# Kernel tuning notes

Hardware: AMD Instinct MI355X
Metric: run time of the kernel (lower is better)

The kernel has to match this reference:

```python
import jax, jax.numpy as jnp
import numpy as np

N = 50000      # nodes
E = 800000     # edges (avg degree 16)
F_IN = 128     # input features
HID = 64       # hidden per head
HEADS = 4      # heads per layer
G = 256        # graphs in batch
C = 10         # classes
ALPHA = 0.01   # leaky relu negative slope


def setup_inputs() -> dict:
    key = jax.random.key(0)
    ks = jax.random.split(key, 12)
    x = jax.random.normal(ks[0], (N, F_IN), dtype=jnp.float32)
    edge_index = jax.random.randint(ks[1], (2, E), 0, N, dtype=jnp.int32)
    batch = jnp.sort(jax.random.randint(ks[2], (N,), 0, G, dtype=jnp.int32))

    def glorot(k, shape):
        fan_in = shape[0] if len(shape) == 2 else int(np.prod(shape[1:]))
        return (jax.random.normal(k, shape, dtype=jnp.float32) / np.float32(np.sqrt(fan_in)))

    W1 = glorot(ks[3], (F_IN, HEADS * HID))
    a1_src = glorot(ks[4], (HEADS, HID))
    a1_dst = glorot(ks[5], (HEADS, HID))
    W2 = glorot(ks[6], (HEADS * HID, HEADS * HID))
    a2_src = glorot(ks[7], (HEADS, HID))
    a2_dst = glorot(ks[8], (HEADS, HID))
    lin_W = glorot(ks[9], (2 * HEADS * HID, C))
    lin_b = jnp.zeros((C,), dtype=jnp.float32)
    return {
        "x": x, "edge_index": edge_index, "batch": batch,
        "W1": W1, "a1_src": a1_src, "a1_dst": a1_dst,
        "W2": W2, "a2_src": a2_src, "a2_dst": a2_dst,
        "lin_W": lin_W, "lin_b": lin_b,
    }


def _gat_layer(x, src, dst, W, a_src, a_dst):
    """Multi-head GAT layer: edge softmax over incoming neighbors, concat heads, ELU."""
    n = x.shape[0]
    h, f = a_src.shape
    Wh = (x @ W).reshape(n, h, f)                       # [N,H,F]
    # per-node attention logits (decomposed GAT attention a^T [Wh_i || Wh_j])
    ls = jnp.einsum("nhf,hf->nh", Wh, a_src)            # [N,H]
    ld = jnp.einsum("nhf,hf->nh", Wh, a_dst)            # [N,H]
    e = jax.nn.leaky_relu(ls[src] + ld[dst], ALPHA)      # [E,H]
    # numerically-stable softmax over edges grouped by destination node
    m = jax.ops.segment_max(e, dst, num_segments=n)      # [N,H]
    m = jnp.where(jnp.isfinite(m), m, 0.0)
    p = jnp.exp(e - m[dst])                              # [E,H]
    z = jax.ops.segment_sum(p, dst, num_segments=n)      # [N,H]
    attn = p / (z[dst] + 1e-16)                          # [E,H]
    msg = Wh[src] * attn[:, :, None]                     # [E,H,F]
    out = jax.ops.segment_sum(msg, dst, num_segments=n)  # [N,H,F]
    return jax.nn.elu(out.reshape(n, h * f))


def reference(x, edge_index, batch, W1, a1_src, a1_dst, W2, a2_src, a2_dst, lin_W, lin_b):
    src, dst = edge_index[0], edge_index[1]
    x = _gat_layer(x, src, dst, W1, a1_src, a1_dst)
    x = _gat_layer(x, src, dst, W2, a2_src, a2_dst)
    # global max / mean pool per graph
    mx = jax.ops.segment_max(x, batch, num_segments=G)
    mx = jnp.where(jnp.isfinite(mx), mx, 0.0)
    s = jax.ops.segment_sum(x, batch, num_segments=G)
    cnt = jax.ops.segment_sum(jnp.ones((x.shape[0], 1), x.dtype), batch, num_segments=G)
    mean = s / jnp.maximum(cnt, 1.0)
    pooled = jnp.concatenate([mx, mean], axis=1)         # [G, 2*H*F]
    return pooled @ lin_W + lin_b                        # [G, C]
```

## Files before the change

### kernel.cpp

```cpp
#include <hip/hip_runtime.h>
#include <hip/hip_bf16.h>

#define NNODES 50000
#define NEDGES 800000
#define FIN    128
#define HID    64
#define HEADS  4
#define NGRAPH 256
#define NCLS   10
#define DTOT   256
#define ALPHA  0.01f
#define CAPLG  6
#define CAP    (1 << CAPLG)

typedef short bf16x8 __attribute__((ext_vector_type(8)));
typedef float f32x4  __attribute__((ext_vector_type(4)));

#define NB      ((NNODES + 255) / 256)
#define EB      ((NEDGES + 255) / 256)
#define XB      ((NNODES * FIN / 4 + 255) / 256)
#define W1B     (FIN * DTOT / 256)
#define W2B     (DTOT * DTOT / 256)

__device__ __forceinline__ ushort f2bf(float v) {
    return __bfloat16_as_ushort(__float2bfloat16(v));
}
__device__ __forceinline__ float blo(unsigned u) { return __uint_as_float(u << 16); }
__device__ __forceinline__ float bhi(unsigned u) { return __uint_as_float(u & 0xffff0000u); }
__device__ __forceinline__ unsigned pack2(float lo, float hi) {
    return ((unsigned)f2bf(hi) << 16) | (unsigned)f2bf(lo);
}

__global__ __launch_bounds__(256) void k_setup(const int* __restrict__ src, const int* __restrict__ dst,
                                               int* __restrict__ cursor, ushort* __restrict__ esrc,
                                               const int* __restrict__ batch, int* __restrict__ gstart,
                                               const float4* __restrict__ x4, ushort4* __restrict__ xbf4,
                                               const float* __restrict__ W1, ushort* __restrict__ W1t,
                                               const float* __restrict__ W2, ushort* __restrict__ W2t) {
    int b = blockIdx.x, t = threadIdx.x;
    if (b < EB) {
        int e = b * 256 + t;
        if (e < NEDGES) {
            int d = dst[e];
            int pos = atomicAdd(&cursor[d], 1);
            if (pos < CAP) esrc[(d << CAPLG) + pos] = (ushort)src[e];
        }
    } else if (b < EB + NB) {
        int i = (b - EB) * 256 + t;
        if (i >= NNODES) return;
        int bb = batch[i];
        if (i == 0) {
            for (int g = 0; g <= bb; ++g) gstart[g] = 0;
        } else {
            int pb = batch[i - 1];
            if (pb != bb) for (int g = pb + 1; g <= bb; ++g) gstart[g] = i;
        }
        if (i == NNODES - 1)
            for (int g = bb + 1; g <= NGRAPH; ++g) gstart[g] = NNODES;
    } else if (b < EB + NB + XB) {
        int i = (b - EB - NB) * 256 + t;
        if (i >= NNODES * FIN / 4) return;
        float4 v = x4[i];
        ushort4 o;
        o.x = f2bf(v.x); o.y = f2bf(v.y); o.z = f2bf(v.z); o.w = f2bf(v.w);
        xbf4[i] = o;
    } else if (b < EB + NB + XB + W1B) {
        int id = (b - EB - NB - XB) * 256 + t;
        int n = id & 255, k = id >> 8;
        W1t[n * FIN + (((k >> 3) ^ (n & 7)) << 3) + (k & 7)] = f2bf(W1[k * DTOT + n]);
    } else {
        int id = (b - EB - NB - XB - W1B) * 256 + t;
        int n = id & 255, k = id >> 8;
        W2t[n * DTOT + (((k >> 3) ^ (n & 7)) << 3) + (k & 7)] = f2bf(W2[k * DTOT + n]);
    }
}

template <int K>
__global__ __launch_bounds__(512) void k_gemm_mfma(const ushort* __restrict__ Abf,
                                                   const ushort* __restrict__ Bt,
                                                   ushort* __restrict__ Cbf,
                                                   float* __restrict__ ls,
                                                   float* __restrict__ ld_,
                                                   const float* __restrict__ a_src,
                                                   const float* __restrict__ a_dst,
                                                   int M) {
    __shared__ ushort Bl[256 * 64];
    const int tid  = threadIdx.x;
    const int w    = tid >> 6;
    const int lane = tid & 63;
    const int l15  = lane & 15;
    const int quad = lane >> 4;
    const int m0 = blockIdx.x * 128;

    f32x4 acc[16];
#pragma unroll
    for (int nf = 0; nf < 16; ++nf) acc[nf] = (f32x4){0.f, 0.f, 0.f, 0.f};

    int rowA0 = m0 + w * 16 + l15;  if (rowA0 >= M) rowA0 = M - 1;
    const ushort* pa0 = Abf + (size_t)rowA0 * K + quad * 8;

#pragma unroll
    for (int kc = 0; kc < K / 64; ++kc) {
        {
#pragma unroll
            for (int idx = tid; idx < 2048; idx += 512) {
                int n = idx >> 3, c8 = (idx ^ n) & 7;
                *(uint4*)&Bl[n * 64 + c8 * 8] =
                    *(const uint4*)&Bt[(size_t)n * K + kc * 64 + c8 * 8];
            }
        }
        __syncthreads();
#pragma unroll
        for (int ks = 0; ks < 2; ++ks) {
            bf16x8 a0 = *(const bf16x8*)(pa0 + kc * 64 + ks * 32);
#pragma unroll
            for (int nh = 0; nh < 4; ++nh) {
                bf16x8 bfr[4];
#pragma unroll
                for (int j = 0; j < 4; ++j) {
                    int n = (nh * 4 + j) * 16 + l15;
                    int c = (ks * 4 + quad) ^ (n & 7);
                    bfr[j] = *(const bf16x8*)&Bl[n * 64 + (c << 3)];
                }
#pragma unroll
                for (int j = 0; j < 4; ++j)
                    acc[nh * 4 + j] = __builtin_amdgcn_mfma_f32_16x16x32_bf16(a0, bfr[j], acc[nh * 4 + j], 0, 0, 0);
            }
        }
        __syncthreads();
    }

    float as[16], ad[16];
#pragma unroll
    for (int nf = 0; nf < 16; ++nf) {
        int head = nf >> 2;
        as[nf] = a_src[head * HID + (nf & 3) * 16 + l15];
        ad[nf] = a_dst[head * HID + (nf & 3) * 16 + l15];
    }
#pragma unroll
    for (int reg = 0; reg < 4; ++reg) {
        int row = m0 + w * 16 + quad * 4 + reg;
        bool ok = row < M;
        if (ok) {
#pragma unroll
            for (int nf = 0; nf < 16; ++nf)
                Cbf[(size_t)row * DTOT + nf * 16 + l15] = f2bf(acc[nf][reg]);
        }
        float sh[4], dh[4];
#pragma unroll
        for (int head = 0; head < 4; ++head) {
            float s = 0.f, d = 0.f;
#pragma unroll
            for (int j = 0; j < 4; ++j) {
                int nf = head * 4 + j;
                s += acc[nf][reg] * as[nf];
                d += acc[nf][reg] * ad[nf];
            }
            sh[head] = s; dh[head] = d;
        }
#pragma unroll
        for (int off = 1; off < 16; off <<= 1) {
#pragma unroll
            for (int head = 0; head < 4; ++head) {
                sh[head] += __shfl_xor(sh[head], off);
                dh[head] += __shfl_xor(dh[head], off);
            }
        }
        if (ok && l15 == 0) {
#pragma unroll
            for (int head = 0; head < 4; ++head) {
                ls[row * HEADS + head]  = sh[head];
                ld_[row * HEADS + head] = dh[head];
            }
        }
    }
}

__global__ __launch_bounds__(256) void k_gat_aggr(const int* __restrict__ cnt,
                                                  const ushort* __restrict__ esrc,
                                                  const ushort* __restrict__ Whbf,
                                                  const float* __restrict__ ls,
                                                  const float* __restrict__ ld_,
                                                  ushort* __restrict__ out) {
    const int wv   = threadIdx.x >> 6;
    const int lane = threadIdx.x & 63;
    const int i    = blockIdx.x * 4 + wv;
    if (i >= NNODES) return;
    const int half = lane >> 5;
    const int l32  = lane & 31;
    const int h    = l32 >> 3;
    const int e0 = i << CAPLG;
    int deg = cnt[i]; if (deg > CAP) deg = CAP;
    const int e1 = e0 + deg;
    const float ldv = ld_[i * HEADS + h];

    float ac[8] = {};
    float z = 0.f;
    const int ch = 8 * l32;
    int e = e0 + half;
    for (; e + 6 < e1; e += 8) {
        int s0 = (int)esrc[e], s1 = (int)esrc[e + 2], s2 = (int)esrc[e + 4], s3 = (int)esrc[e + 6];
        float l0 = ls[s0 * HEADS + h] + ldv;
        float l1 = ls[s1 * HEADS + h] + ldv;
        float l2 = ls[s2 * HEADS + h] + ldv;
        float l3 = ls[s3 * HEADS + h] + ldv;
        uint4 u0 = *(const uint4*)&Whbf[(size_t)s0 * DTOT + ch];
        uint4 u1 = *(const uint4*)&Whbf[(size_t)s1 * DTOT + ch];
        uint4 u2 = *(const uint4*)&Whbf[(size_t)s2 * DTOT + ch];
        uint4 u3 = *(const uint4*)&Whbf[(size_t)s3 * DTOT + ch];
        float p0 = __expf(l0 > 0.f ? l0 : ALPHA * l0);
        float p1 = __expf(l1 > 0.f ? l1 : ALPHA * l1);
        float p2 = __expf(l2 > 0.f ? l2 : ALPHA * l2);
        float p3 = __expf(l3 > 0.f ? l3 : ALPHA * l3);
        z += p0 + p1 + p2 + p3;
        ac[0] = fmaf(p0, blo(u0.x), ac[0]); ac[1] = fmaf(p0, bhi(u0.x), ac[1]);
        ac[2] = fmaf(p0, blo(u0.y), ac[2]); ac[3] = fmaf(p0, bhi(u0.y), ac[3]);
        ac[4] = fmaf(p0, blo(u0.z), ac[4]); ac[5] = fmaf(p0, bhi(u0.z), ac[5]);
        ac[6] = fmaf(p0, blo(u0.w), ac[6]); ac[7] = fmaf(p0, bhi(u0.w), ac[7]);
        ac[0] = fmaf(p1, blo(u1.x), ac[0]); ac[1] = fmaf(p1, bhi(u1.x), ac[1]);
        ac[2] = fmaf(p1, blo(u1.y), ac[2]); ac[3] = fmaf(p1, bhi(u1.y), ac[3]);
        ac[4] = fmaf(p1, blo(u1.z), ac[4]); ac[5] = fmaf(p1, bhi(u1.z), ac[5]);
        ac[6] = fmaf(p1, blo(u1.w), ac[6]); ac[7] = fmaf(p1, bhi(u1.w), ac[7]);
        ac[0] = fmaf(p2, blo(u2.x), ac[0]); ac[1] = fmaf(p2, bhi(u2.x), ac[1]);
        ac[2] = fmaf(p2, blo(u2.y), ac[2]); ac[3] = fmaf(p2, bhi(u2.y), ac[3]);
        ac[4] = fmaf(p2, blo(u2.z), ac[4]); ac[5] = fmaf(p2, bhi(u2.z), ac[5]);
        ac[6] = fmaf(p2, blo(u2.w), ac[6]); ac[7] = fmaf(p2, bhi(u2.w), ac[7]);
        ac[0] = fmaf(p3, blo(u3.x), ac[0]); ac[1] = fmaf(p3, bhi(u3.x), ac[1]);
        ac[2] = fmaf(p3, blo(u3.y), ac[2]); ac[3] = fmaf(p3, bhi(u3.y), ac[3]);
        ac[4] = fmaf(p3, blo(u3.z), ac[4]); ac[5] = fmaf(p3, bhi(u3.z), ac[5]);
        ac[6] = fmaf(p3, blo(u3.w), ac[6]); ac[7] = fmaf(p3, bhi(u3.w), ac[7]);
    }
    for (; e < e1; e += 2) {
        int s0 = (int)esrc[e];
        float l0 = ls[s0 * HEADS + h] + ldv;
        uint4 u0 = *(const uint4*)&Whbf[(size_t)s0 * DTOT + ch];
        float p0 = __expf(l0 > 0.f ? l0 : ALPHA * l0);
        z += p0;
        ac[0] = fmaf(p0, blo(u0.x), ac[0]); ac[1] = fmaf(p0, bhi(u0.x), ac[1]);
        ac[2] = fmaf(p0, blo(u0.y), ac[2]); ac[3] = fmaf(p0, bhi(u0.y), ac[3]);
        ac[4] = fmaf(p0, blo(u0.z), ac[4]); ac[5] = fmaf(p0, bhi(u0.z), ac[5]);
        ac[6] = fmaf(p0, blo(u0.w), ac[6]); ac[7] = fmaf(p0, bhi(u0.w), ac[7]);
    }

#pragma unroll
    for (int j = 0; j < 8; ++j) ac[j] += __shfl_xor(ac[j], 32);
    z += __shfl_xor(z, 32);

    if (half == 0) {
        const float inv = 1.f / (z + 1e-16f);
        float v[8];
#pragma unroll
        for (int j = 0; j < 8; ++j) {
            float t = ac[j] * inv;
            v[j] = t > 0.f ? t : __expf(t) - 1.f;
        }
        uint4 pk;
        pk.x = pack2(v[0], v[1]);
        pk.y = pack2(v[2], v[3]);
        pk.z = pack2(v[4], v[5]);
        pk.w = pack2(v[6], v[7]);
        *(uint4*)(out + (size_t)i * DTOT + ch) = pk;
    }
}

__global__ __launch_bounds__(1024) void k_pool_final(const ushort* __restrict__ h2bf,
                                                     const int* __restrict__ gstart,
                                                     const float* __restrict__ W,
                                                     const float* __restrict__ b,
                                                     float* __restrict__ out) {
    __shared__ float smx[16][256];
    __shared__ float ssm[16][256];
    __shared__ float pooled[2 * DTOT];
    int g = blockIdx.x, t = threadIdx.x;
    int cg = t & 31, j = t >> 5;
    int s = gstart[g], e = gstart[g + 1];
    float mx[8], sm[8];
#pragma unroll
    for (int k = 0; k < 8; ++k) { mx[k] = -INFINITY; sm[k] = 0.f; }
    for (int n = s + j; n < e; n += 32) {
        uint4 u = *(const uint4*)&h2bf[(size_t)n * DTOT + cg * 8];
        float v0 = blo(u.x), v1 = bhi(u.x), v2 = blo(u.y), v3 = bhi(u.y);
        float v4 = blo(u.z), v5 = bhi(u.z), v6 = blo(u.w), v7 = bhi(u.w);
        mx[0] = fmaxf(mx[0], v0); sm[0] += v0;
        mx[1] = fmaxf(mx[1], v1); sm[1] += v1;
        mx[2] = fmaxf(mx[2], v2); sm[2] += v2;
        mx[3] = fmaxf(mx[3], v3); sm[3] += v3;
        mx[4] = fmaxf(mx[4], v4); sm[4] += v4;
        mx[5] = fmaxf(mx[5], v5); sm[5] += v5;
        mx[6] = fmaxf(mx[6], v6); sm[6] += v6;
        mx[7] = fmaxf(mx[7], v7); sm[7] += v7;
    }
#pragma unroll
    for (int k = 0; k < 8; ++k) {
        mx[k] = fmaxf(mx[k], __shfl_xor(mx[k], 32));
        sm[k] += __shfl_xor(sm[k], 32);
    }
    int wave = t >> 6, lane = t & 63;
    if (lane < 32) {
        *(float4*)&smx[wave][lane * 8]     = make_float4(mx[0], mx[1], mx[2], mx[3]);
        *(float4*)&smx[wave][lane * 8 + 4] = make_float4(mx[4], mx[5], mx[6], mx[7]);
        *(float4*)&ssm[wave][lane * 8]     = make_float4(sm[0], sm[1], sm[2], sm[3]);
        *(float4*)&ssm[wave][lane * 8 + 4] = make_float4(sm[4], sm[5], sm[6], sm[7]);
    }
    __syncthreads();
    if (t < 256) {
        float m = -INFINITY, su = 0.f;
#pragma unroll
        for (int jj = 0; jj < 16; ++jj) {
            m = fmaxf(m, smx[jj][t]);
            su += ssm[jj][t];
        }
        int cnt = e - s;
        if (cnt <= 0) m = 0.f;
        pooled[t] = m;
        pooled[DTOT + t] = su / (float)(cnt > 0 ? cnt : 1);
    }
    __syncthreads();
    int wv = t >> 6;
    if (wv < NCLS) {
        float acc = 0.f;
        for (int k = lane; k < 2 * DTOT; k += 64)
            acc += pooled[k] * W[k * NCLS + wv];
#pragma unroll
        for (int off = 32; off; off >>= 1) acc += __shfl_down(acc, off);
        if (lane == 0)
            out[g * NCLS + wv] = acc + b[wv];
    }
}

extern "C" void kernel_launch(void* const* d_in, const int* in_sizes, int n_in,
                              void* d_out, int out_size, void* d_ws, size_t ws_size,
                              hipStream_t stream) {
    const float* x     = (const float*)d_in[0];
    const int*   ei    = (const int*)d_in[1];
    const int*   batch = (const int*)d_in[2];
    const float* W1    = (const float*)d_in[3];
    const float* a1s   = (const float*)d_in[4];
    const float* a1d   = (const float*)d_in[5];
    const float* W2    = (const float*)d_in[6];
    const float* a2s   = (const float*)d_in[7];
    const float* a2d   = (const float*)d_in[8];
    const float* linW  = (const float*)d_in[9];
    const float* linb  = (const float*)d_in[10];
    float* out = (float*)d_out;

    const int* src = ei;
    const int* dst = ei + NEDGES;

    size_t off = 0;
    char* base = (char*)d_ws;
    auto alloc = [&](size_t bytes) -> void* {
        void* p = base + off;
        off += (bytes + 255) & ~(size_t)255;
        return p;
    };
    ushort* xbf    = (ushort*)alloc((size_t)NNODES * FIN * 2);
    ushort* Whbf   = (ushort*)alloc((size_t)NNODES * DTOT * 2);
    ushort* h1bf   = (ushort*)alloc((size_t)NNODES * DTOT * 2);
    ushort* h2bf   = (ushort*)alloc((size_t)NNODES * DTOT * 2);
    float*  ls     = (float*)alloc((size_t)NNODES * HEADS * 4);
    float*  ld_    = (float*)alloc((size_t)NNODES * HEADS * 4);
    int*    cursor = (int*)alloc((size_t)NNODES * 4);
    ushort* esrc   = (ushort*)alloc((size_t)(NNODES << CAPLG) * 2);
    int*    gstart = (int*)alloc((size_t)(NGRAPH + 1) * 4);
    ushort* W1t    = (ushort*)alloc((size_t)DTOT * FIN * 2);
    ushort* W2t    = (ushort*)alloc((size_t)DTOT * DTOT * 2);

    hipMemsetAsync(cursor, 0, (size_t)NNODES * 4, stream);

    int setup_blocks = EB + NB + XB + W1B + W2B;
    k_setup<<<setup_blocks, 256, 0, stream>>>(src, dst, cursor, esrc, batch, gstart,
                                              (const float4*)x, (ushort4*)xbf,
                                              W1, W1t, W2, W2t);

    int ggrid = (NNODES + 127) / 128;

    k_gemm_mfma<FIN><<<ggrid, 512, 0, stream>>>(xbf, W1t, Whbf, ls, ld_, a1s, a1d, NNODES);
    k_gat_aggr<<<(NNODES + 3) / 4, 256, 0, stream>>>(cursor, esrc, Whbf, ls, ld_, h1bf);

    k_gemm_mfma<DTOT><<<ggrid, 512, 0, stream>>>(h1bf, W2t, Whbf, ls, ld_, a2s, a2d, NNODES);
    k_gat_aggr<<<(NNODES + 3) / 4, 256, 0, stream>>>(cursor, esrc, Whbf, ls, ld_, h2bf);

    k_pool_final<<<NGRAPH, 1024, 0, stream>>>(h2bf, gstart, linW, linb, out);
}
```

Baseline: 305.6 us.

## Fuse x fp32-to-bf16 conversion into GEMM and double-buffer B tiles

Drops the separate x-to-bf16 conversion pass from the setup kernel. The first GEMM now reads fp32 x directly and converts it to bf16 in registers, which removes a 25.6 MB read and a 12.8 MB write/re-read round trip. The GEMM also double-buffers the B tile in LDS, prefetching the next K chunk into registers during the MFMAs, so one barrier per chunk is removed. The cost is double the LDS use (64 KB per block) and a launch_bounds hint of 4 blocks, which may reduce occupancy.

```diff
diff --git a/kernel.cpp b/kernel.cpp
--- a/kernel.cpp
+++ b/kernel.cpp
@@ -18,7 +18,6 @@
 
 #define NB      ((NNODES + 255) / 256)
 #define EB      ((NEDGES + 255) / 256)
-#define XB      ((NNODES * FIN / 4 + 255) / 256)
 #define W1B     (FIN * DTOT / 256)
 #define W2B     (DTOT * DTOT / 256)
 
@@ -30,11 +29,18 @@
 __device__ __forceinline__ unsigned pack2(float lo, float hi) {
     return ((unsigned)f2bf(hi) << 16) | (unsigned)f2bf(lo);
 }
+__device__ __forceinline__ bf16x8 cvt8(float4 lo, float4 hi) {
+    bf16x8 r;
+    r[0] = (short)f2bf(lo.x); r[1] = (short)f2bf(lo.y);
+    r[2] = (short)f2bf(lo.z); r[3] = (short)f2bf(lo.w);
+    r[4] = (short)f2bf(hi.x); r[5] = (short)f2bf(hi.y);
+    r[6] = (short)f2bf(hi.z); r[7] = (short)f2bf(hi.w);
+    return r;
+}
 
 __global__ __launch_bounds__(256) void k_setup(const int* __restrict__ src, const int* __restrict__ dst,
                                                int* __restrict__ cursor, ushort* __restrict__ esrc,
                                                const int* __restrict__ batch, int* __restrict__ gstart,
-                                               const float4* __restrict__ x4, ushort4* __restrict__ xbf4,
                                                const float* __restrict__ W1, ushort* __restrict__ W1t,
                                                const float* __restrict__ W2, ushort* __restrict__ W2t) {
     int b = blockIdx.x, t = threadIdx.x;
@@ -57,34 +63,28 @@
         }
         if (i == NNODES - 1)
             for (int g = bb + 1; g <= NGRAPH; ++g) gstart[g] = NNODES;
-    } else if (b < EB + NB + XB) {
-        int i = (b - EB - NB) * 256 + t;
-        if (i >= NNODES * FIN / 4) return;
-        float4 v = x4[i];
-        ushort4 o;
-        o.x = f2bf(v.x); o.y = f2bf(v.y); o.z = f2bf(v.z); o.w = f2bf(v.w);
-        xbf4[i] = o;
-    } else if (b < EB + NB + XB + W1B) {
-        int id = (b - EB - NB - XB) * 256 + t;
+    } else if (b < EB + NB + W1B) {
+        int id = (b - EB - NB) * 256 + t;
         int n = id & 255, k = id >> 8;
         W1t[n * FIN + (((k >> 3) ^ (n & 7)) << 3) + (k & 7)] = f2bf(W1[k * DTOT + n]);
     } else {
-        int id = (b - EB - NB - XB - W1B) * 256 + t;
+        int id = (b - EB - NB - W1B) * 256 + t;
         int n = id & 255, k = id >> 8;
         W2t[n * DTOT + (((k >> 3) ^ (n & 7)) << 3) + (k & 7)] = f2bf(W2[k * DTOT + n]);
     }
 }
 
-template <int K>
-__global__ __launch_bounds__(512) void k_gemm_mfma(const ushort* __restrict__ Abf,
-                                                   const ushort* __restrict__ Bt,
-                                                   ushort* __restrict__ Cbf,
-                                                   float* __restrict__ ls,
-                                                   float* __restrict__ ld_,
-                                                   const float* __restrict__ a_src,
-                                                   const float* __restrict__ a_dst,
-                                                   int M) {
-    __shared__ ushort Bl[256 * 64];
+template <int K, bool AF32>
+__global__ __launch_bounds__(512, 4) void k_gemm_mfma(const void* __restrict__ Aptr,
+                                                      const ushort* __restrict__ Bt,
+                                                      ushort* __restrict__ Cbf,
+                                                      float* __restrict__ ls,
+                                                      float* __restrict__ ld_,
+                                                      const float* __restrict__ a_src,
+                                                      const float* __restrict__ a_dst,
+                                                      int M) {
+    constexpr int NC = K / 64;
+    __shared__ ushort Bl[2][256 * 64];
     const int tid  = threadIdx.x;
     const int w    = tid >> 6;
     const int lane = tid & 63;
@@ -97,22 +97,45 @@
     for (int nf = 0; nf < 16; ++nf) acc[nf] = (f32x4){0.f, 0.f, 0.f, 0.f};
 
     int rowA0 = m0 + w * 16 + l15;  if (rowA0 >= M) rowA0 = M - 1;
-    const ushort* pa0 = Abf + (size_t)rowA0 * K + quad * 8;
-
-#pragma unroll
-    for (int kc = 0; kc < K / 64; ++kc) {
-        {
-#pragma unroll
-            for (int idx = tid; idx < 2048; idx += 512) {
+    const ushort* pa0b = (const ushort*)Aptr + (size_t)rowA0 * K + quad * 8;
+    const float*  pa0f = (const float*)Aptr  + (size_t)rowA0 * K + quad * 8;
+
+    uint4 rg[4];
+#pragma unroll
+    for (int it = 0; it < 4; ++it) {
+        int idx = tid + it * 512;
+        int n = idx >> 3, c8 = (idx ^ n) & 7;
+        rg[it] = *(const uint4*)&Bt[(size_t)n * K + c8 * 8];
+    }
+#pragma unroll
+    for (int it = 0; it < 4; ++it) {
+        int idx = tid + it * 512;
+        int n = idx >> 3, c8 = (idx ^ n) & 7;
+        *(uint4*)&Bl[0][n * 64 + c8 * 8] = rg[it];
+    }
+    __syncthreads();
+
+#pragma unroll
+    for (int kc = 0; kc < NC; ++kc) {
+        if (kc + 1 < NC) {
+#pragma unroll
+            for (int it = 0; it < 4; ++it) {
+                int idx = tid + it * 512;
                 int n = idx >> 3, c8 = (idx ^ n) & 7;
-                *(uint4*)&Bl[n * 64 + c8 * 8] =
-                    *(const uint4*)&Bt[(size_t)n * K + kc * 64 + c8 * 8];
-            }
-        }
-        __syncthreads();
+                rg[it] = *(const uint4*)&Bt[(size_t)n * K + (kc + 1) * 64 + c8 * 8];
+            }
+        }
 #pragma unroll
         for (int ks = 0; ks < 2; ++ks) {
-            bf16x8 a0 = *(const bf16x8*)(pa0 + kc * 64 + ks * 32);
+            bf16x8 a0;
+            if constexpr (AF32) {
+                const float* p = pa0f + kc * 64 + ks * 32;
+                float4 alo = *(const float4*)p;
+                float4 ahi = *(const float4*)(p + 4);
+                a0 = cvt8(alo, ahi);
+            } else {
+                a0 = *(const bf16x8*)(pa0b + kc * 64 + ks * 32);
+            }
 #pragma unroll
             for (int nh = 0; nh < 4; ++nh) {
                 bf16x8 bfr[4];
@@ -120,11 +143,19 @@
                 for (int j = 0; j < 4; ++j) {
                     int n = (nh * 4 + j) * 16 + l15;
                     int c = (ks * 4 + quad) ^ (n & 7);
-                    bfr[j] = *(const bf16x8*)&Bl[n * 64 + (c << 3)];
+                    bfr[j] = *(const bf16x8*)&Bl[kc & 1][n * 64 + (c << 3)];
                 }
 #pragma unroll
                 for (int j = 0; j < 4; ++j)
                     acc[nh * 4 + j] = __builtin_amdgcn_mfma_f32_16x16x32_bf16(a0, bfr[j], acc[nh * 4 + j], 0, 0, 0);
+            }
+        }
+        if (kc + 1 < NC) {
+#pragma unroll
+            for (int it = 0; it < 4; ++it) {
+                int idx = tid + it * 512;
+                int n = idx >> 3, c8 = (idx ^ n) & 7;
+                *(uint4*)&Bl[(kc + 1) & 1][n * 64 + c8 * 8] = rg[it];
             }
         }
         __syncthreads();
@@ -354,7 +385,6 @@
         off += (bytes + 255) & ~(size_t)255;
         return p;
     };
-    ushort* xbf    = (ushort*)alloc((size_t)NNODES * FIN * 2);
     ushort* Whbf   = (ushort*)alloc((size_t)NNODES * DTOT * 2);
     ushort* h1bf   = (ushort*)alloc((size_t)NNODES * DTOT * 2);
     ushort* h2bf   = (ushort*)alloc((size_t)NNODES * DTOT * 2);
@@ -368,17 +398,16 @@
 
     hipMemsetAsync(cursor, 0, (size_t)NNODES * 4, stream);
 
-    int setup_blocks = EB + NB + XB + W1B + W2B;
+    int setup_blocks = EB + NB + W1B + W2B;
     k_setup<<<setup_blocks, 256, 0, stream>>>(src, dst, cursor, esrc, batch, gstart,
-                                              (const float4*)x, (ushort4*)xbf,
                                               W1, W1t, W2, W2t);
 
     int ggrid = (NNODES + 127) / 128;
 
-    k_gemm_mfma<FIN><<<ggrid, 512, 0, stream>>>(xbf, W1t, Whbf, ls, ld_, a1s, a1d, NNODES);
+    k_gemm_mfma<FIN, true><<<ggrid, 512, 0, stream>>>((const void*)x, W1t, Whbf, ls, ld_, a1s, a1d, NNODES);
     k_gat_aggr<<<(NNODES + 3) / 4, 256, 0, stream>>>(cursor, esrc, Whbf, ls, ld_, h1bf);
 
-    k_gemm_mfma<DTOT><<<ggrid, 512, 0, stream>>>(h1bf, W2t, Whbf, ls, ld_, a2s, a2d, NNODES);
+    k_gemm_mfma<DTOT, false><<<ggrid, 512, 0, stream>>>((const void*)h1bf, W2t, Whbf, ls, ld_, a2s, a2d, NNODES);
     k_gat_aggr<<<(NNODES + 3) / 4, 256, 0, stream>>>(cursor, esrc, Whbf, ls, ld_, h2bf);
 
     k_pool_final<<<NGRAPH, 1024, 0, stream>>>(h2bf, gstart, linW, linb, out);
```

Measured after the change: 321.3 us. +5.2%, slower.
